# Kernel tuning notes

Measured on AMD Instinct MI355X. Metric: run time of the kernel, lower is better.

## Reference

```python
import jax, jax.numpy as jnp
import numpy as np
from jax import lax

D = 48  # cfg.MAX_DISP // 4 with MAX_DISP = 192


def conv2d(x, w, stride=1):
    return lax.conv_general_dilated(x, w, (stride, stride), [(1, 1), (1, 1)],
                                    dimension_numbers=('NCHW', 'OIHW', 'NCHW'))


def conv3d(x, w):
    return lax.conv_general_dilated(x, w, (1, 1, 1), [(1, 1)] * 3,
                                    dimension_numbers=('NCDHW', 'OIDHW', 'NCDHW'))


def bn(x, s, b):
    # eval-mode BatchNorm folded into per-channel scale/bias
    shape = (1, -1) + (1,) * (x.ndim - 2)
    return x * s.reshape(shape) + b.reshape(shape)


def encoder(x, p):
    x = jax.nn.relu(bn(conv2d(x, p['e_w1'], 2), p['e_s1'], p['e_b1']))
    x = jax.nn.relu(bn(conv2d(x, p['e_w2'], 1), p['e_s2'], p['e_b2']))
    x = jax.nn.relu(bn(conv2d(x, p['e_w3'], 2), p['e_s3'], p['e_b3']))
    x = jax.nn.relu(bn(conv2d(x, p['e_w4'], 1), p['e_s4'], p['e_b4']))
    return x  # [B, 32, H/4, W/4]


def build_corr(fl, fr):
    # cost[b, d, h, w] = mean_c fl[b,c,h,w] * fr[b,c,h,w-d], zero where w < d
    B, C, H, W = fl.shape
    padded = jnp.pad(fr, ((0, 0), (0, 0), (0, 0), (D - 1, 0)))  # zero-pad left

    def body(_, d):
        r = lax.dynamic_slice(padded, (0, 0, 0, D - 1 - d), (B, C, H, W))
        return None, jnp.mean(fl * r, axis=1)

    _, cost = lax.scan(body, None, jnp.arange(D))  # [D, B, H, W]
    return jnp.transpose(cost, (1, 0, 2, 3))  # [B, D, H, W]


def forward(img_l, img_r, p):
    H, W = img_l.shape[2], img_l.shape[3]
    fl = encoder(img_l, p)
    fr = encoder(img_r, p)
    cost = build_corr(fl, fr)
    # 3D cost aggregation: treat cost as [B, 1, D, h, w]
    x = cost[:, None]
    x = jax.nn.relu(bn(conv3d(x, p['a_w1']), p['a_s1'], p['a_b1']))
    x = jax.nn.relu(bn(conv3d(x, p['a_w2']), p['a_s2'], p['a_b2']))
    cost = conv3d(x, p['a_w3'])[:, 0]  # [B, D, h, w]
    prob = jax.nn.softmax(-cost, axis=1)
    idx = jnp.arange(D, dtype=cost.dtype).reshape(1, D, 1, 1)
    disp_low = jnp.sum(prob * idx, axis=1, keepdims=True)  # [B, 1, h, w]
    # upsample (bilinear, align_corners=False semantics) and refine
    disp = jax.image.resize(disp_low, (disp_low.shape[0], 1, H, W), method='bilinear') * 4.0
    disp = jax.nn.relu(bn(conv2d(disp, p['r_w1']), p['r_s1'], p['r_b1']))
    disp = jax.nn.relu(conv2d(disp, p['r_w2']))
    return disp, fl


def setup_inputs() -> dict:
    key = jax.random.key(0)
    ks = jax.random.split(key, 32)
    B, H, W = 4, 384, 768

    def n(k, shape, scale=0.1):
        return jax.random.normal(k, shape, jnp.float32) * scale

    inp = {
        'img_l': n(ks[0], (B, 3, H, W), 1.0),
        'img_r': n(ks[1], (B, 3, H, W), 1.0),
        'e_w1': n(ks[2], (16, 3, 3, 3)),
        'e_w2': n(ks[3], (16, 16, 3, 3)),
        'e_w3': n(ks[4], (32, 16, 3, 3)),
        'e_w4': n(ks[5], (32, 32, 3, 3)),
        'e_s1': 1.0 + n(ks[6], (16,)),
        'e_s2': 1.0 + n(ks[7], (16,)),
        'e_s3': 1.0 + n(ks[8], (32,)),
        'e_s4': 1.0 + n(ks[9], (32,)),
        'e_b1': n(ks[10], (16,)),
        'e_b2': n(ks[11], (16,)),
        'e_b3': n(ks[12], (32,)),
        'e_b4': n(ks[13], (32,)),
        'a_w1': n(ks[14], (8, 1, 3, 3, 3)),
        'a_s1': 1.0 + n(ks[15], (8,)),
        'a_b1': n(ks[16], (8,)),
        'a_w2': n(ks[17], (16, 8, 3, 3, 3)),
        'a_s2': 1.0 + n(ks[18], (16,)),
        'a_b2': n(ks[19], (16,)),
        'a_w3': n(ks[20], (1, 16, 3, 3, 3)),
        'r_w1': n(ks[21], (16, 1, 3, 3)),
        'r_s1': 1.0 + n(ks[22], (16,)),
        'r_b1': n(ks[23], (16,)),
        'r_w2': n(ks[24], (1, 16, 3, 3)),
    }
    return inp


def reference(img_l, img_r, e_w1, e_w2, e_w3, e_w4, e_s1, e_s2, e_s3, e_s4,
              e_b1, e_b2, e_b3, e_b4, a_w1, a_s1, a_b1, a_w2, a_s2, a_b2,
              a_w3, r_w1, r_s1, r_b1, r_w2):
    p = dict(e_w1=e_w1, e_w2=e_w2, e_w3=e_w3, e_w4=e_w4,
             e_s1=e_s1, e_s2=e_s2, e_s3=e_s3, e_s4=e_s4,
             e_b1=e_b1, e_b2=e_b2, e_b3=e_b3, e_b4=e_b4,
             a_w1=a_w1, a_s1=a_s1, a_b1=a_b1, a_w2=a_w2, a_s2=a_s2,
             a_b2=a_b2, a_w3=a_w3, r_w1=r_w1, r_s1=r_s1, r_b1=r_b1,
             r_w2=r_w2)
    return forward(img_l, img_r, p)
```

## Files before the change

### kernel.cpp

```cpp
#include <hip/hip_runtime.h>
#include <hip/hip_bf16.h>

typedef __hip_bfloat16 bf16;
typedef __attribute__((ext_vector_type(8))) short short8v;
typedef __attribute__((ext_vector_type(4))) float f32x4;

static inline int cdiv(long long a, int b){ return (int)((a + b - 1) / b); }

__device__ __forceinline__ float uaf(unsigned u){ return __uint_as_float(u); }
__device__ __forceinline__ float ldf(const bf16* p){ return __bfloat162float(*p); }
__device__ __forceinline__ void stf(bf16* p, float v){ *p = __float2bfloat16(v); }

__device__ __forceinline__ void load4v(const float* p, float& a, float& b, float& c, float& d){
    float4 v = *reinterpret_cast<const float4*>(p); a = v.x; b = v.y; c = v.z; d = v.w;
}
__device__ __forceinline__ unsigned short bfbits(float v){
    bf16 h = __float2bfloat16(v); unsigned short s; __builtin_memcpy(&s, &h, 2); return s;
}

__global__ void halo2d_k(bf16* buf, long long bstride, int nsub, long long sstride,
                         int Hp, int Wp, int Cv)
{
    int z = blockIdx.z;
    bf16* b = buf + (long long)(z / nsub) * bstride + (long long)(z % nsub) * sstride;
    uint4 zz = make_uint4(0, 0, 0, 0);
    int rowV = Wp * Cv;
    int totalV = 2 * rowV + (Hp - 2) * 2 * Cv;
    for (int i = blockIdx.x * 256 + threadIdx.x; i < totalV; i += gridDim.x * 256) {
        long long off;
        if (i < rowV) off = i;
        else if (i < 2 * rowV) off = (long long)(Hp - 1) * rowV + (i - rowV);
        else {
            int k = i - 2 * rowV;
            int h = 1 + k / (2 * Cv);
            int r = k % (2 * Cv);
            int wc = (r < Cv) ? 0 : (Wp - 1);
            off = (long long)h * rowV + (long long)wc * Cv + (r < Cv ? r : r - Cv);
        }
        reinterpret_cast<uint4*>(b)[off] = zz;
    }
}

__global__ void zero_planes_k(bf16* buf, long long bstride, long long planeV, int lastPlane)
{
    int b = blockIdx.z, p = blockIdx.y;
    uint4 zz = make_uint4(0, 0, 0, 0);
    bf16* base = buf + (long long)b * bstride;
    long long pl = p ? (long long)lastPlane * planeV : 0;
    for (long long i = blockIdx.x * 256 + threadIdx.x; i < planeV; i += (long long)gridDim.x * 256)
        reinterpret_cast<uint4*>(base)[pl + i] = zz;
}

#define E12_BS 2396288LL
#define E3_BS  1216768LL

__global__ __launch_bounds__(256) void conv_e1(
    const float* __restrict__ in0, const float* __restrict__ in1,
    const float* __restrict__ w, const float* __restrict__ sc, const float* __restrict__ bi,
    bf16* __restrict__ out)
{
    const int H = 384, W = 768, NW = 96;
    int img = blockIdx.z;
    const float* in = (img >= 4) ? in1 + (long long)(img - 4) * 3 * 294912
                                 : in0 + (long long)img * 3 * 294912;

    __shared__ float wl[432];
    __shared__ float sl[16], bl[16];
    for (int j = threadIdx.x; j < 432; j += 256) {
        int k = j / 16, o = j % 16;
        wl[j] = w[o * 27 + k];
    }
    if (threadIdx.x < 16) { sl[threadIdx.x] = sc[threadIdx.x]; bl[threadIdx.x] = bi[threadIdx.x]; }
    __syncthreads();

    int unit = blockIdx.x * 256 + threadIdx.x;
    int h = unit / NW, wseg = unit % NW, w0 = wseg << 2;
    const long long HW = (long long)H * W;

    float acc[16][4];
#pragma unroll
    for (int o = 0; o < 16; ++o){ acc[o][0]=0.f; acc[o][1]=0.f; acc[o][2]=0.f; acc[o][3]=0.f; }

    for (int ic = 0; ic < 3; ++ic) {
        const float* ip = in + (long long)ic * HW;
#pragma unroll
        for (int kh = 0; kh < 3; ++kh) {
            int ih = 2 * h + kh - 1;
            if (ih < 0 || ih >= H) continue;
            const float* row = ip + (long long)ih * W;
            float x0,x1,x2,x3,x4,x5,x6,x7;
            load4v(row + 2 * w0,     x0, x1, x2, x3);
            load4v(row + 2 * w0 + 4, x4, x5, x6, x7);
            float xm = (w0 > 0) ? row[2 * w0 - 1] : 0.f;
            const float* wk = wl + (ic * 9 + kh * 3) * 16;
#pragma unroll
            for (int o = 0; o < 16; ++o) {
                float wa = wk[o], wb = wk[16 + o], wc = wk[32 + o];
                acc[o][0] = fmaf(xm, wa, fmaf(x0, wb, fmaf(x1, wc, acc[o][0])));
                acc[o][1] = fmaf(x1, wa, fmaf(x2, wb, fmaf(x3, wc, acc[o][1])));
                acc[o][2] = fmaf(x3, wa, fmaf(x4, wb, fmaf(x5, wc, acc[o][2])));
                acc[o][3] = fmaf(x5, wa, fmaf(x6, wb, fmaf(x7, wc, acc[o][3])));
            }
        }
    }
    char* ob = (char*)out + (long long)img * E12_BS;
#pragma unroll
    for (int i = 0; i < 4; ++i) {
        float v[16];
#pragma unroll
        for (int o = 0; o < 16; ++o) v[o] = fmaxf(acc[o][i] * sl[o] + bl[o], 0.f);
        uint4 u0, u1;
        u0.x = (unsigned)bfbits(v[0])  | ((unsigned)bfbits(v[1])  << 16);
        u0.y = (unsigned)bfbits(v[2])  | ((unsigned)bfbits(v[3])  << 16);
        u0.z = (unsigned)bfbits(v[4])  | ((unsigned)bfbits(v[5])  << 16);
        u0.w = (unsigned)bfbits(v[6])  | ((unsigned)bfbits(v[7])  << 16);
        u1.x = (unsigned)bfbits(v[8])  | ((unsigned)bfbits(v[9])  << 16);
        u1.y = (unsigned)bfbits(v[10]) | ((unsigned)bfbits(v[11]) << 16);
        u1.z = (unsigned)bfbits(v[12]) | ((unsigned)bfbits(v[13]) << 16);
        u1.w = (unsigned)bfbits(v[14]) | ((unsigned)bfbits(v[15]) << 16);
        char* p = ob + ((long long)(h + 1) * 386 + (w0 + i + 1)) * 32;
        *reinterpret_cast<uint4*>(p)      = u0;
        *reinterpret_cast<uint4*>(p + 16) = u1;
    }
}

__global__ __launch_bounds__(256) void conv_e2_mfma(
    const bf16* __restrict__ in, const float* __restrict__ w,
    const float* __restrict__ sc, const float* __restrict__ bi,
    bf16* __restrict__ out)
{
    __shared__ short alds[16 * 160];
    __shared__ int offl[20];
    int tid = threadIdx.x;
    for (int j = tid; j < 16 * 160; j += 256) {
        int oc = j / 160, kk = j % 160;
        short v = 0;
        if (kk < 144) { int tap = kk / 16, ic = kk % 16; v = (short)bfbits(w[oc * 144 + ic * 9 + tap]); }
        alds[j] = v;
    }
    if (tid < 20) {
        int c = tid / 4, g = tid % 4;
        int tap = 2 * c + (g >> 1); if (tap > 8) tap = 8;
        offl[tid] = ((tap / 3) * 386 + (tap % 3)) * 32 + (g & 1) * 16;
    }
    __syncthreads();

    int wid = tid >> 6, lane = tid & 63;
    int wt = blockIdx.x * 4 + wid;
    int h = wt / 6, w0 = (wt % 6) * 64;
    int img = blockIdx.z;
    int g = lane >> 4, px = lane & 15;

    const char* bp = (const char*)in + (long long)img * E12_BS
                   + ((long long)h * 386 + (w0 + px)) * 32;
    int offr[5];
#pragma unroll
    for (int c = 0; c < 5; ++c) offr[c] = offl[c * 4 + g];
    short8v af[5];
#pragma unroll
    for (int c = 0; c < 5; ++c)
        af[c] = *reinterpret_cast<const short8v*>(&alds[px * 160 + 32 * c + 8 * g]);

    f32x4 acc[4];
#pragma unroll
    for (int pg = 0; pg < 4; ++pg) {
        f32x4 a = {0.f, 0.f, 0.f, 0.f};
        const char* bpp = bp + pg * 512;
#pragma unroll
        for (int c = 0; c < 5; ++c) {
            short8v bf = *reinterpret_cast<const short8v*>(bpp + offr[c]);
            a = __builtin_amdgcn_mfma_f32_16x16x32_bf16(af[c], bf, a, 0, 0, 0);
        }
        acc[pg] = a;
    }
    char* ob = (char*)out + (long long)img * E12_BS;
#pragma unroll
    for (int pg = 0; pg < 4; ++pg) {
        float v[4];
#pragma unroll
        for (int r = 0; r < 4; ++r) {
            int oc = g * 4 + r;
            v[r] = fmaxf(acc[pg][r] * sc[oc] + bi[oc], 0.f);
        }
        uint2 u;
        u.x = (unsigned)bfbits(v[0]) | ((unsigned)bfbits(v[1]) << 16);
        u.y = (unsigned)bfbits(v[2]) | ((unsigned)bfbits(v[3]) << 16);
        *reinterpret_cast<uint2*>(ob + ((long long)(h + 1) * 386 + (w0 + pg * 16 + px + 1)) * 32 + g * 8) = u;
    }
}

__global__ __launch_bounds__(256) void conv_e3_mfma(
    const bf16* __restrict__ in, const float* __restrict__ w,
    const float* __restrict__ sc, const float* __restrict__ bi,
    bf16* __restrict__ out)
{
    __shared__ short alds[16 * 160];
    __shared__ int offl[20];
    int tid = threadIdx.x;
    int och = blockIdx.y;
    for (int j = tid; j < 16 * 160; j += 256) {
        int oc = j / 160, kk = j % 160;
        short v = 0;
        if (kk < 144) { int tap = kk / 16, ic = kk % 16; v = (short)bfbits(w[(och * 16 + oc) * 144 + ic * 9 + tap]); }
        alds[j] = v;
    }
    if (tid < 20) {
        int c = tid / 4, g = tid % 4;
        int tap = 2 * c + (g >> 1); if (tap > 8) tap = 8;
        offl[tid] = ((tap / 3) * 386 + (tap % 3)) * 32 + (g & 1) * 16;
    }
    __syncthreads();

    int wid = tid >> 6, lane = tid & 63;
    int wt = blockIdx.x * 4 + wid;
    int h = wt / 3, w0 = (wt % 3) * 64;
    int img = blockIdx.z;
    int g = lane >> 4, px = lane & 15;

    const char* bp = (const char*)in + (long long)img * E12_BS
                   + ((long long)(2 * h) * 386 + 2 * (w0 + px)) * 32;
    int offr[5];
#pragma unroll
    for (int c = 0; c < 5; ++c) offr[c] = offl[c * 4 + g];
    short8v af[5];
#pragma unroll
    for (int c = 0; c < 5; ++c)
        af[c] = *reinterpret_cast<const short8v*>(&alds[px * 160 + 32 * c + 8 * g]);

    f32x4 acc[4];
#pragma unroll
    for (int pg = 0; pg < 4; ++pg) {
        f32x4 a = {0.f, 0.f, 0.f, 0.f};
        const char* bpp = bp + pg * 1024;
#pragma unroll
        for (int c = 0; c < 5; ++c) {
            short8v bf = *reinterpret_cast<const short8v*>(bpp + offr[c]);
            a = __builtin_amdgcn_mfma_f32_16x16x32_bf16(af[c], bf, a, 0, 0, 0);
        }
        acc[pg] = a;
    }
    char* ob = (char*)out + (long long)img * E3_BS;
#pragma unroll
    for (int pg = 0; pg < 4; ++pg) {
        float v[4];
#pragma unroll
        for (int r = 0; r < 4; ++r) {
            int oc = och * 16 + g * 4 + r;
            v[r] = fmaxf(acc[pg][r] * sc[oc] + bi[oc], 0.f);
        }
        uint2 u;
        u.x = (unsigned)bfbits(v[0]) | ((unsigned)bfbits(v[1]) << 16);
        u.y = (unsigned)bfbits(v[2]) | ((unsigned)bfbits(v[3]) << 16);
        *reinterpret_cast<uint2*>(ob + ((long long)(h + 1) * 194 + (w0 + pg * 16 + px + 1)) * 64
                                  + och * 32 + g * 8) = u;
    }
}

__global__ __launch_bounds__(256) void conv_e4_mfma(
    const bf16* __restrict__ in, const float* __restrict__ w,
    const float* __restrict__ sc, const float* __restrict__ bi,
    float* __restrict__ fl, float* __restrict__ fr)
{
    __shared__ short alds[16 * 288];
    __shared__ int offl[36];
    int tid = threadIdx.x;
    int och = blockIdx.y;
    for (int j = tid; j < 16 * 288; j += 256) {
        int oc = j / 288, kk = j % 288;
        int tap = kk / 32, ic = kk % 32;
        alds[j] = (short)bfbits(w[(och * 16 + oc) * 288 + ic * 9 + tap]);
    }
    if (tid < 36) {
        int c = tid / 4, g = tid % 4;
        offl[tid] = ((c / 3) * 194 + (c % 3)) * 64 + g * 16;
    }
    __syncthreads();

    int wid = tid >> 6, lane = tid & 63;
    int wt = blockIdx.x * 4 + wid;
    int h = wt / 3, w0 = (wt % 3) * 64;
    int img = blockIdx.z;
    int g = lane >> 4, px = lane & 15;

    const char* bp = (const char*)in + (long long)img * E3_BS
                   + ((long long)h * 194 + (w0 + px)) * 64;
    int offr[9];
#pragma unroll
    for (int c = 0; c < 9; ++c) offr[c] = offl[c * 4 + g];
    short8v af[9];
#pragma unroll
    for (int c = 0; c < 9; ++c)
        af[c] = *reinterpret_cast<const short8v*>(&alds[px * 288 + 32 * c + 8 * g]);

    f32x4 acc[4];
#pragma unroll
    for (int pg = 0; pg < 4; ++pg) {
        f32x4 a = {0.f, 0.f, 0.f, 0.f};
        const char* bpp = bp + pg * 1024;
#pragma unroll
        for (int c = 0; c < 9; ++c) {
            short8v bf = *reinterpret_cast<const short8v*>(bpp + offr[c]);
            a = __builtin_amdgcn_mfma_f32_16x16x32_bf16(af[c], bf, a, 0, 0, 0);
        }
        acc[pg] = a;
    }
    float* dst = (img < 4) ? fl + (long long)img * 32 * 18432
                           : fr + (long long)(img - 4) * 32 * 18432;
#pragma unroll
    for (int pg = 0; pg < 4; ++pg) {
#pragma unroll
        for (int r = 0; r < 4; ++r) {
            int oc = och * 16 + g * 4 + r;
            float v = fmaxf(acc[pg][r] * sc[oc] + bi[oc], 0.f);
            dst[(long long)oc * 18432 + (long long)h * 192 + w0 + pg * 16 + px] = v;
        }
    }
}

#define PB1E 7604800LL
#define PB2E 15209600LL

__global__ __launch_bounds__(256) void conv1_nhwc(
    const float* __restrict__ in, const float* __restrict__ w,
    const float* __restrict__ sc, const float* __restrict__ bi,
    bf16* __restrict__ out)
{
    const int H = 96, W = 192, D = 48, NW = 48;
    int zb = blockIdx.z;
    const float* inz = in + (long long)zb * 884736;
    bf16* outz = out + (long long)zb * PB1E;
    int d = blockIdx.y;
    __shared__ float wl[216];
    __shared__ float sl[8], bl[8];
    for (int j = threadIdx.x; j < 216; j += 256) wl[j] = w[j];
    if (threadIdx.x < 8) { sl[threadIdx.x] = sc[threadIdx.x]; bl[threadIdx.x] = bi[threadIdx.x]; }
    __syncthreads();

    int unit = blockIdx.x * 256 + threadIdx.x;
    int h = unit / NW, wseg = unit % NW, w0 = wseg << 2;
    if (h >= H) return;

    float acc[8][4];
#pragma unroll
    for (int o = 0; o < 8; ++o){ acc[o][0]=0.f; acc[o][1]=0.f; acc[o][2]=0.f; acc[o][3]=0.f; }

#pragma unroll
    for (int kd = 0; kd < 3; ++kd) {
        int id = d + kd - 1;
        if (id < 0 || id >= D) continue;
        const float* plane = inz + (long long)id * H * W;
#pragma unroll
        for (int kh = 0; kh < 3; ++kh) {
            int ih = h + kh - 1;
            if (ih < 0 || ih >= H) continue;
            const float* row = plane + (long long)ih * W;
            float x0,x1,x2,x3;
            load4v(row + w0, x0, x1, x2, x3);
            float xl = (wseg > 0)      ? row[w0 - 1] : 0.f;
            float xr = (wseg < NW - 1) ? row[w0 + 4] : 0.f;
            int kb = kd * 9 + kh * 3;
#pragma unroll
            for (int o = 0; o < 8; ++o) {
                float wa = wl[o*27 + kb], wb = wl[o*27 + kb + 1], wc = wl[o*27 + kb + 2];
                acc[o][0] = fmaf(xl, wa, fmaf(x0, wb, fmaf(x1, wc, acc[o][0])));
                acc[o][1] = fmaf(x0, wa, fmaf(x1, wb, fmaf(x2, wc, acc[o][1])));
                acc[o][2] = fmaf(x1, wa, fmaf(x2, wb, fmaf(x3, wc, acc[o][2])));
                acc[o][3] = fmaf(x2, wa, fmaf(x3, wb, fmaf(xr, wc, acc[o][3])));
            }
        }
    }
#pragma unroll
    for (int i = 0; i < 4; ++i) {
        uint4 u;
        float v[8];
#pragma unroll
        for (int o = 0; o < 8; ++o) v[o] = fmaxf(acc[o][i] * sl[o] + bl[o], 0.f);
        u.x = (unsigned)bfbits(v[0]) | ((unsigned)bfbits(v[1]) << 16);
        u.y = (unsigned)bfbits(v[2]) | ((unsigned)bfbits(v[3]) << 16);
        u.z = (unsigned)bfbits(v[4]) | ((unsigned)bfbits(v[5]) << 16);
        u.w = (unsigned)bfbits(v[6]) | ((unsigned)bfbits(v[7]) << 16);
        long long idx = (((long long)(d + 1) * 98 + (h + 1)) * 194 + (w0 + 1 + i)) * 8;
        *reinterpret_cast<uint4*>(&outz[idx]) = u;
    }
}

__global__ __launch_bounds__(256) void conv2_mfma(
    const bf16* __restrict__ in, const float* __restrict__ w,
    const float* __restrict__ sc, const float* __restrict__ bi,
    bf16* __restrict__ out)
{
    __shared__ short alds[16 * 224];
    __shared__ uint4 sB[6 * 3 * 66];
    __shared__ int offl[28];
    int tid = threadIdx.x;
    int zb = blockIdx.z;
    const bf16* inz = in + (long long)zb * PB1E;
    for (int j = tid; j < 16 * 224; j += 256) {
        int oc = j / 224, kk = j % 224;
        short v = 0;
        if (kk < 216) { int t = kk / 8, ic = kk % 8; v = (short)bfbits(w[(oc * 8 + ic) * 27 + t]); }
        alds[j] = v;
    }
    if (tid < 28) {
        int t = (tid < 27) ? tid : 26;
        int kd = t / 9, kh = (t / 3) % 3, kw = t % 3;
        offl[tid] = (kd * 3 + kh) * 66 + kw;
    }

    int hw = blockIdx.x;
    int h = hw / 3, w0 = (hw % 3) * 64;
    int dq = blockIdx.y * 4;
    for (int j = tid; j < 1188; j += 256) {
        int p = j / 198, rem = j % 198;
        int r = rem / 66, c = rem % 66;
        sB[j] = *reinterpret_cast<const uint4*>(
            inz + (((long long)(dq + p) * 98 + (h + r)) * 194 + (w0 + c)) * 8);
    }
    __syncthreads();

    int wid = tid >> 6, lane = tid & 63;
    int g = lane >> 4, px = lane & 15;
    int d = dq + wid;

    const uint4* sBw = sB + wid * 198;
    int offr[7];
#pragma unroll
    for (int c = 0; c < 7; ++c) offr[c] = offl[4 * c + g];
    short8v af[7];
#pragma unroll
    for (int c = 0; c < 7; ++c)
        af[c] = *reinterpret_cast<const short8v*>(&alds[px * 224 + 32 * c + 8 * g]);

    f32x4 acc[4];
#pragma unroll
    for (int pg = 0; pg < 4; ++pg) {
        f32x4 a = {0.f, 0.f, 0.f, 0.f};
        int col = pg * 16 + px;
#pragma unroll
        for (int c = 0; c < 7; ++c) {
            short8v bf = *reinterpret_cast<const short8v*>(&sBw[offr[c] + col]);
            a = __builtin_amdgcn_mfma_f32_16x16x32_bf16(af[c], bf, a, 0, 0, 0);
        }
        acc[pg] = a;
    }

    char* ob = (char*)(out + (long long)zb * PB2E);
#pragma unroll
    for (int pg = 0; pg < 4; ++pg) {
        float v[4];
#pragma unroll
        for (int r = 0; r < 4; ++r) {
            int oc = g * 4 + r;
            v[r] = fmaxf(acc[pg][r] * sc[oc] + bi[oc], 0.f);
        }
        long long pxi = ((long long)(d + 1) * 98 + h + 1) * 194 + (w0 + pg * 16 + px + 1);
        uint2 u;
        u.x = (unsigned)bfbits(v[0]) | ((unsigned)bfbits(v[1]) << 16);
        u.y = (unsigned)bfbits(v[2]) | ((unsigned)bfbits(v[3]) << 16);
        *reinterpret_cast<uint2*>(ob + pxi * 32 + g * 8) = u;
    }
}

__global__ __launch_bounds__(256) void conv3_mfma(
    const bf16* __restrict__ in, const float* __restrict__ w,
    float* __restrict__ out)
{
    __shared__ uint4 sB[6 * 4 * 66 * 2];
    __shared__ short wlds[448] __attribute__((aligned(16)));
    __shared__ int offl[56];
    int tid = threadIdx.x;
    int zb = blockIdx.z;
    const bf16* inz = in + (long long)zb * PB2E;

    for (int j = tid; j < 448; j += 256) {
        int t = j / 16, ic = j % 16;
        wlds[j] = (t < 27) ? (short)bfbits(w[ic * 27 + t]) : (short)0;
    }
    if (tid < 56) {
        int c = tid / 4, g = tid % 4;
        int t = 2 * c + (g >> 1); if (t > 26) t = 26;
        int off = ((t / 9) * 4 + (t / 3) % 3) * 66 + (t % 3);
        offl[tid] = off * 2 + (g & 1);
    }

    int hw = blockIdx.x;
    int h0 = (hw / 3) * 2, w0 = (hw % 3) * 64;
    int dq = blockIdx.y * 4;
    const uint4* src = reinterpret_cast<const uint4*>(inz);
    for (int j = tid; j < 3168; j += 256) {
        int half = j & 1, pxl = j >> 1;
        int p = pxl / 264, rem = pxl % 264;
        int r = rem / 66, c = rem % 66;
        sB[j] = src[(((long long)(dq + p) * 98 + (h0 + r)) * 194 + (w0 + c)) * 2 + half];
    }
    __syncthreads();

    int wid = tid >> 6, lane = tid & 63;
    int g = lane >> 4, pxi = lane & 15;
    const uint4* sBw = sB + wid * 528;

    int offr[14];
#pragma unroll
    for (int c = 0; c < 14; ++c) offr[c] = offl[c * 4 + g];
    short8v af[14];
    short8v zv = {0,0,0,0,0,0,0,0};
#pragma unroll
    for (int c = 0; c < 14; ++c)
        af[c] = (pxi == 0) ? *reinterpret_cast<const short8v*>(&wlds[32 * c + 8 * g]) : zv;

    f32x4 acc[2][4];
#pragma unroll
    for (int rr = 0; rr < 2; ++rr) {
#pragma unroll
        for (int pg = 0; pg < 4; ++pg) {
            f32x4 a = {0.f, 0.f, 0.f, 0.f};
            int pcol = (pg * 16 + pxi) * 2 + rr * 132;
#pragma unroll
            for (int c = 0; c < 14; ++c) {
                short8v bf = *reinterpret_cast<const short8v*>(&sBw[offr[c] + pcol]);
                a = __builtin_amdgcn_mfma_f32_16x16x32_bf16(af[c], bf, a, 0, 0, 0);
            }
            acc[rr][pg] = a;
        }
    }

    float* outz = out + (long long)zb * 884736;
    if (lane < 16) {
#pragma unroll
        for (int rr = 0; rr < 2; ++rr) {
            long long base = ((long long)(dq + wid) * 96 + h0 + rr) * 192 + w0 + lane;
#pragma unroll
            for (int pg = 0; pg < 4; ++pg)
                outz[base + pg * 16] = acc[rr][pg][0];
        }
    }
}

__global__ __launch_bounds__(256) void corr2_k(
    const float* __restrict__ fl, const float* __restrict__ fr,
    float* __restrict__ cost)
{
    const int C = 32, D = 48, H = 96, W = 192;
    __shared__ float sfl[64 * 33];
    __shared__ float sfr[111 * 33];

    int w0 = blockIdx.x * 64, h = blockIdx.y, b = blockIdx.z;
    int tid = threadIdx.x;

    for (int j = tid; j < 64 * C; j += 256) {
        int w = j % 64, c = j / 64;
        sfl[w * 33 + c] = fl[(((long long)b * C + c) * H + h) * W + w0 + w];
    }
    for (int j = tid; j < 111 * C; j += 256) {
        int wp = j % 111, c = j / 111;
        int gw = w0 - 47 + wp;
        sfr[wp * 33 + c] = (gw >= 0) ? fr[(((long long)b * C + c) * H + h) * W + gw] : 0.f;
    }
    __syncthreads();

    int w = tid & 63, dg = tid >> 6;
    float flr[32];
#pragma unroll
    for (int c = 0; c < 32; ++c) flr[c] = sfl[w * 33 + c];

    for (int dd = 0; dd < 12; ++dd) {
        int d = dg * 12 + dd;
        int wi = w - d + 47;
        float a = 0.f;
#pragma unroll
        for (int c = 0; c < 32; ++c) a = fmaf(flr[c], sfr[wi * 33 + c], a);
        cost[(((long long)b * D + d) * H + h) * W + w0 + w] = a * (1.0f / 32.0f);
    }
}

__global__ void softdisp_k(const float* __restrict__ c3, float* __restrict__ dl,
                           int B, int H, int W)
{
    const int D = 48;
    long long idx = (long long)blockIdx.x * blockDim.x + threadIdx.x;
    long long total = (long long)B * H * W;
    if (idx >= total) return;
    int b = (int)(idx / ((long long)H * W));
    long long rem = idx % ((long long)H * W);
    const float* p = c3 + ((long long)b * D) * H * W + rem;
    long long st = (long long)H * W;

    float v[48];
    float mn = 1e30f;
#pragma unroll
    for (int d = 0; d < D; ++d) { v[d] = p[d * st]; mn = fminf(mn, v[d]); }
    float se = 0.f, sd = 0.f;
#pragma unroll
    for (int d = 0; d < D; ++d) {
        float e = expf(mn - v[d]);
        se += e;
        sd += e * (float)d;
    }
    dl[idx] = sd / se;
}

__global__ __launch_bounds__(256) void refine_fused(
    const float* __restrict__ dlow, const float* __restrict__ w1,
    const float* __restrict__ s1, const float* __restrict__ b1,
    const float* __restrict__ w2, float* __restrict__ out)
{
    const int H = 384, W = 768, Hl = 96, Wl = 192;
    __shared__ float sdu[20][21];
    __shared__ float smid[18][18][20];
    __shared__ float w1l[144], s1l[16], b1l[16], w2l[144];
    int tid = threadIdx.x;
    if (tid < 144) {
        w1l[tid] = w1[tid];
        int ic = tid / 9, tap = tid % 9;
        w2l[tap * 16 + ic] = w2[tid];
    } else if (tid < 160) {
        s1l[tid - 144] = s1[tid - 144]; b1l[tid - 144] = b1[tid - 144];
    }

    int b = blockIdx.z, h0 = blockIdx.y * 16, w0 = blockIdx.x * 16;
    const float* dlb = dlow + (long long)b * Hl * Wl;
    for (int j = tid; j < 400; j += 256) {
        int i = j / 20, k = j % 20;
        int y = h0 - 2 + i, x = w0 - 2 + k;
        float v = 0.f;
        if (y >= 0 && y < H && x >= 0 && x < W) {
            float sy = (y + 0.5f) * 0.25f - 0.5f;
            float sx = (x + 0.5f) * 0.25f - 0.5f;
            sy = fminf(fmaxf(sy, 0.f), (float)(Hl - 1));
            sx = fminf(fmaxf(sx, 0.f), (float)(Wl - 1));
            int y0 = (int)sy, x0 = (int)sx;
            int y1 = min(y0 + 1, Hl - 1), x1 = min(x0 + 1, Wl - 1);
            float fy = sy - y0, fx = sx - x0;
            v = 4.0f * ((1.f - fy) * ((1.f - fx) * dlb[y0 * Wl + x0] + fx * dlb[y0 * Wl + x1])
                      +        fy  * ((1.f - fx) * dlb[y1 * Wl + x0] + fx * dlb[y1 * Wl + x1]));
        }
        sdu[i][k] = v;
    }
    __syncthreads();

    for (int idx = tid; idx < 324; idx += 256) {
        int i = idx / 18, j = idx % 18;
        int gy = h0 - 1 + i, gx = w0 - 1 + j;
        bool inimg = (gy >= 0 && gy < H && gx >= 0 && gx < W);
        float t[9];
#pragma unroll
        for (int kh = 0; kh < 3; ++kh)
#pragma unroll
            for (int kw = 0; kw < 3; ++kw) t[kh * 3 + kw] = sdu[i + kh][j + kw];
        float m[16];
#pragma unroll
        for (int oc = 0; oc < 16; ++oc) {
            float s = 0.f;
#pragma unroll
            for (int k = 0; k < 9; ++k) s = fmaf(t[k], w1l[oc * 9 + k], s);
            m[oc] = inimg ? fmaxf(s * s1l[oc] + b1l[oc], 0.f) : 0.f;
        }
#pragma unroll
        for (int q = 0; q < 4; ++q)
            *reinterpret_cast<float4*>(&smid[i][j][q * 4]) =
                make_float4(m[q*4], m[q*4+1], m[q*4+2], m[q*4+3]);
    }
    __syncthreads();

    int i = tid >> 4, j = tid & 15;
    float s = 0.f;
#pragma unroll
    for (int kh = 0; kh < 3; ++kh)
#pragma unroll
        for (int kw = 0; kw < 3; ++kw) {
            const float* mp = &smid[i + kh][j + kw][0];
            const float* wp = &w2l[(kh * 3 + kw) * 16];
#pragma unroll
            for (int q = 0; q < 4; ++q) {
                float4 x = *reinterpret_cast<const float4*>(mp + q * 4);
                s = fmaf(x.x, wp[q*4+0], s);
                s = fmaf(x.y, wp[q*4+1], s);
                s = fmaf(x.z, wp[q*4+2], s);
                s = fmaf(x.w, wp[q*4+3], s);
            }
        }
    out[(long long)b * H * W + (long long)(h0 + i) * W + w0 + j] = fmaxf(s, 0.f);
}

extern "C" void kernel_launch(void* const* d_in, const int* in_sizes, int n_in,
                              void* d_out, int out_size, void* d_ws, size_t ws_size,
                              hipStream_t stream)
{
    const float* img_l = (const float*)d_in[0];
    const float* img_r = (const float*)d_in[1];
    const float* e_w1 = (const float*)d_in[2];
    const float* e_w2 = (const float*)d_in[3];
    const float* e_w3 = (const float*)d_in[4];
    const float* e_w4 = (const float*)d_in[5];
    const float* e_s1 = (const float*)d_in[6];
    const float* e_s2 = (const float*)d_in[7];
    const float* e_s3 = (const float*)d_in[8];
    const float* e_s4 = (const float*)d_in[9];
    const float* e_b1 = (const float*)d_in[10];
    const float* e_b2 = (const float*)d_in[11];
    const float* e_b3 = (const float*)d_in[12];
    const float* e_b4 = (const float*)d_in[13];
    const float* a_w1 = (const float*)d_in[14];
    const float* a_s1 = (const float*)d_in[15];
    const float* a_b1 = (const float*)d_in[16];
    const float* a_w2 = (const float*)d_in[17];
    const float* a_s2 = (const float*)d_in[18];
    const float* a_b2 = (const float*)d_in[19];
    const float* a_w3 = (const float*)d_in[20];
    const float* r_w1 = (const float*)d_in[21];
    const float* r_s1 = (const float*)d_in[22];
    const float* r_b1 = (const float*)d_in[23];
    const float* r_w2 = (const float*)d_in[24];

    const int B = 4, H = 384, W = 768, H4 = 96, W4 = 192, D = 48;
    const long long HW4 = (long long)H4 * W4;
    const long long DHW = (long long)D * HW4;
    const long long E12E = E12_BS / 2;
    const long long P1E = 98LL * 194 * 8;
    const long long P2E = 98LL * 194 * 16;

    float* out_disp = (float*)d_out;
    float* FL       = out_disp + 1179648;

    char* ws = (char*)d_ws;
    bf16*  E1pad = (bf16*)(ws + 0);
    bf16*  E2pad = (bf16*)(ws + 19170304);
    bf16*  E3pad = (bf16*)(ws + 38340608);
    float* FR    = (float*)(ws + 48074752);
    float* COST  = (float*)(ws + 0);
    bf16*  C1pad = (bf16*) (ws + 14155776);
    bf16*  C2pad = (bf16*) (ws + 44574976);
    float* C3    = COST;
    float* DL    = (float*)(ws + 166251776);

    dim3 blk(256);

    halo2d_k<<<dim3(10, 1, 16), blk, 0, stream>>>(E1pad, E12E, 1, 0, 194, 386, 2);
    halo2d_k<<<dim3(10, 1, 8),  blk, 0, stream>>>(E3pad, E3_BS / 2, 1, 0, 98, 194, 4);

    conv_e1<<<dim3(72, 1, 8), blk, 0, stream>>>(img_l, img_r, e_w1, e_s1, e_b1, E1pad);
    conv_e2_mfma<<<dim3(288, 1, 8), blk, 0, stream>>>(E1pad, e_w2, e_s2, e_b2, E2pad);
    conv_e3_mfma<<<dim3(72, 2, 8), blk, 0, stream>>>(E2pad, e_w3, e_s3, e_b3, E3pad);
    conv_e4_mfma<<<dim3(72, 2, 8), blk, 0, stream>>>(E3pad, e_w4, e_s4, e_b4, FL, FR);

    corr2_k<<<dim3(3, 96, 4), blk, 0, stream>>>(FL, FR, COST);

    zero_planes_k<<<dim3(75, 2, 2), blk, 0, stream>>>(C1pad, PB1E, P1E / 8, 49);
    halo2d_k<<<dim3(3, 1, 96), blk, 0, stream>>>(C1pad + P1E, PB1E, 48, P1E, 98, 194, 1);
    zero_planes_k<<<dim3(75, 2, 4), blk, 0, stream>>>(C2pad, PB2E, P2E / 8, 49);
    halo2d_k<<<dim3(5, 1, 192), blk, 0, stream>>>(C2pad + P2E, PB2E, 48, P2E, 98, 194, 2);

    for (int sb = 0; sb < 2; ++sb) {
        conv1_nhwc<<<dim3(18, 48, 2), blk, 0, stream>>>(
            COST + sb * 2 * DHW, a_w1, a_s1, a_b1, C1pad);
        conv2_mfma<<<dim3(288, 12, 2), blk, 0, stream>>>(
            C1pad, a_w2, a_s2, a_b2, C2pad + sb * 2 * PB2E);
    }

    conv3_mfma<<<dim3(144, 12, 4), blk, 0, stream>>>(C2pad, a_w3, C3);

    softdisp_k<<<cdiv(4LL*H4*W4, 256), blk, 0, stream>>>(C3, DL, B, H4, W4);

    refine_fused<<<dim3(48, 24, 4), blk, 0, stream>>>(
        DL, r_w1, r_s1, r_b1, r_w2, out_disp);
}
```

Before: 372.1 us.

## Use full MFMA rows in conv3 by mapping four disparity outputs to A matrix

The final 3D conv (16->1 channel) previously used only one row of each 16x16 MFMA A operand, with the other rows zero, wasting most of the matrix work. It now builds a banded weight matrix in LDS so that four output disparity planes share one MFMA, over a 6-plane K window of 864 taps. Each wave covers 16 pixel columns instead of 64, and the MFMA count per block falls. The cost is a larger LDS weight table built per block, 27 A fragments held in registers, and output writes scattered across disparity planes.

```diff
diff --git a/kernel.cpp b/kernel.cpp
--- a/kernel.cpp
+++ b/kernel.cpp
@@ -466,21 +466,29 @@
     float* __restrict__ out)
 {
     __shared__ uint4 sB[6 * 4 * 66 * 2];
-    __shared__ short wlds[448] __attribute__((aligned(16)));
-    __shared__ int offl[56];
+    __shared__ short aT[16 * 868] __attribute__((aligned(16)));
+    __shared__ int offl[108];
     int tid = threadIdx.x;
     int zb = blockIdx.z;
     const bf16* inz = in + (long long)zb * PB2E;
 
-    for (int j = tid; j < 448; j += 256) {
-        int t = j / 16, ic = j % 16;
-        wlds[j] = (t < 27) ? (short)bfbits(w[ic * 27 + t]) : (short)0;
-    }
-    if (tid < 56) {
+    for (int j = tid; j < 16 * 868; j += 256) {
+        int m = j / 868, k = j % 868;
+        short v = 0;
+        if (k < 864) {
+            int ch = k & 15, T = k >> 4;
+            int p = T / 9, t9 = T % 9;
+            int rel = p - m;
+            if (rel >= 0 && rel <= 2) v = (short)bfbits(w[ch * 27 + rel * 9 + t9]);
+        }
+        aT[j] = v;
+    }
+    if (tid < 108) {
         int c = tid / 4, g = tid % 4;
-        int t = 2 * c + (g >> 1); if (t > 26) t = 26;
-        int off = ((t / 9) * 4 + (t / 3) % 3) * 66 + (t % 3);
-        offl[tid] = off * 2 + (g & 1);
+        int T = 2 * c + (g >> 1);
+        int p = T / 9, t9 = T % 9;
+        int kh = t9 / 3, kw = t9 % 3;
+        offl[tid] = ((p * 4 + kh) * 66 + kw) * 2 + (g & 1);
     }
 
     int hw = blockIdx.x;
@@ -496,42 +504,37 @@
     __syncthreads();
 
     int wid = tid >> 6, lane = tid & 63;
-    int g = lane >> 4, pxi = lane & 15;
-    const uint4* sBw = sB + wid * 528;
-
-    int offr[14];
-#pragma unroll
-    for (int c = 0; c < 14; ++c) offr[c] = offl[c * 4 + g];
-    short8v af[14];
-    short8v zv = {0,0,0,0,0,0,0,0};
-#pragma unroll
-    for (int c = 0; c < 14; ++c)
-        af[c] = (pxi == 0) ? *reinterpret_cast<const short8v*>(&wlds[32 * c + 8 * g]) : zv;
-
-    f32x4 acc[2][4];
+    int g = lane >> 4, col = lane & 15;
+
+    int offr[27];
+#pragma unroll
+    for (int c = 0; c < 27; ++c) offr[c] = offl[c * 4 + g] + (wid * 16 + col) * 2;
+    short8v af[27];
+#pragma unroll
+    for (int c = 0; c < 27; ++c)
+        af[c] = *reinterpret_cast<const short8v*>(&aT[col * 868 + c * 32 + g * 8]);
+
+    f32x4 acc[2];
 #pragma unroll
     for (int rr = 0; rr < 2; ++rr) {
-#pragma unroll
-        for (int pg = 0; pg < 4; ++pg) {
-            f32x4 a = {0.f, 0.f, 0.f, 0.f};
-            int pcol = (pg * 16 + pxi) * 2 + rr * 132;
-#pragma unroll
-            for (int c = 0; c < 14; ++c) {
-                short8v bf = *reinterpret_cast<const short8v*>(&sBw[offr[c] + pcol]);
-                a = __builtin_amdgcn_mfma_f32_16x16x32_bf16(af[c], bf, a, 0, 0, 0);
-            }
-            acc[rr][pg] = a;
-        }
+        f32x4 a = {0.f, 0.f, 0.f, 0.f};
+        int radd = rr * 132;
+#pragma unroll
+        for (int c = 0; c < 27; ++c) {
+            short8v bf = *reinterpret_cast<const short8v*>(&sB[offr[c] + radd]);
+            a = __builtin_amdgcn_mfma_f32_16x16x32_bf16(af[c], bf, a, 0, 0, 0);
+        }
+        acc[rr] = a;
     }
 
     float* outz = out + (long long)zb * 884736;
     if (lane < 16) {
 #pragma unroll
         for (int rr = 0; rr < 2; ++rr) {
-            long long base = ((long long)(dq + wid) * 96 + h0 + rr) * 192 + w0 + lane;
-#pragma unroll
-            for (int pg = 0; pg < 4; ++pg)
-                outz[base + pg * 16] = acc[rr][pg][0];
+#pragma unroll
+            for (int r = 0; r < 4; ++r) {
+                outz[((long long)(dq + r) * 96 + h0 + rr) * 192 + w0 + wid * 16 + lane] = acc[rr][r];
+            }
         }
     }
 }
```

After: 468.2 us. 25.8% more time.
